# Kernel optimization log

Hardware: AMD Instinct MI355X
Metric: run time of the kernel (lower is better)

The kernel has to match this reference:

```python
import jax, jax.numpy as jnp
import numpy as np

VOCAB, ENC, EMB, DEC, ATT = 10000, 2048, 512, 512, 512
B, P, S = 64, 196, 20
PAD_ID = 0


def setup_inputs() -> dict:
    key = jax.random.key(0)
    ks = jax.random.split(key, 20)
    sc = lambda *sh: 1.0 / np.sqrt(sh[-1])
    def lin(k, out, inp):
        kw, kb = jax.random.split(k)
        s = 1.0 / np.sqrt(inp)
        return (jax.random.uniform(kw, (out, inp), jnp.float32, -s, s),
                jax.random.uniform(kb, (out,), jnp.float32, -s, s))
    wenc_w, wenc_b = lin(ks[0], ATT, ENC)
    wdec_w, wdec_b = lin(ks[1], ATT, DEC)
    V_w, V_b = lin(ks[2], 1, ATT)
    h0_w, h0_b = lin(ks[3], DEC, ENC)
    c0_w, c0_b = lin(ks[4], DEC, ENC)
    W_ih, b_ih = lin(ks[5], 4 * DEC, ENC + EMB)
    W_hh, b_hh = lin(ks[6], 4 * DEC, DEC)
    fc_w, fc_b = lin(ks[7], VOCAB, DEC)
    embed_w = jax.random.normal(ks[8], (VOCAB, EMB), jnp.float32)
    embed_w = embed_w.at[PAD_ID].set(0.0)  # padding_idx row is zero
    image_feat = jax.random.normal(ks[9], (B, P, ENC), jnp.float32)
    captions_ids = jax.random.randint(ks[10], (B, S), 0, VOCAB)
    return dict(image_feat=image_feat, captions_ids=captions_ids,
                wenc_w=wenc_w, wenc_b=wenc_b, wdec_w=wdec_w, wdec_b=wdec_b,
                V_w=V_w, V_b=V_b, embed_w=embed_w,
                h0_w=h0_w, h0_b=h0_b, c0_w=c0_w, c0_b=c0_b,
                W_ih=W_ih, b_ih=b_ih, W_hh=W_hh, b_hh=b_hh,
                fc_w=fc_w, fc_b=fc_b)


def reference(image_feat, captions_ids, wenc_w, wenc_b, wdec_w, wdec_b,
              V_w, V_b, embed_w, h0_w, h0_b, c0_w, c0_b,
              W_ih, b_ih, W_hh, b_hh, fc_w, fc_b):
    # eval mode: no input noise, dropout = identity
    avg = image_feat.mean(axis=1)                                   # [B, ENC]
    h = jax.nn.relu(avg @ h0_w.T + h0_b)                            # [B, DEC]
    c = jax.nn.relu(avg @ c0_w.T + c0_b)
    enc_proj = jnp.einsum('bpe,ae->bpa', image_feat, wenc_w) + wenc_b  # [B,P,ATT]
    emb_seq = embed_w[captions_ids]                                 # [B,S,EMB]
    emb_seq = jnp.transpose(emb_seq, (1, 0, 2))                     # [S,B,EMB]

    def step(carry, emb_t):
        h, c = carry
        att = jnp.tanh(enc_proj + (h @ wdec_w.T + wdec_b)[:, None, :])  # [B,P,ATT]
        e = jnp.einsum('bpa,a->bp', att, V_w[0]) + V_b[0]               # [B,P]
        w = jax.nn.softmax(e, axis=1)
        ctx = jnp.einsum('bp,bpe->be', w, image_feat)                   # [B,ENC]
        x = jnp.concatenate([ctx, emb_t], axis=1)                       # [B,ENC+EMB]
        gates = x @ W_ih.T + b_ih + h @ W_hh.T + b_hh                   # [B,4*DEC]
        i, f, g, o = jnp.split(gates, 4, axis=1)
        c_new = jax.nn.sigmoid(f) * c + jax.nn.sigmoid(i) * jnp.tanh(g)
        h_new = jax.nn.sigmoid(o) * jnp.tanh(c_new)
        logits = h_new @ fc_w.T + fc_b                                  # [B,VOCAB]
        return (h_new, c_new), logits

    _, preds = jax.lax.scan(step, (h, c), emb_seq)                  # [S,B,VOCAB]
    return jnp.transpose(preds, (1, 0, 2))                          # [B,S,VOCAB]
```

## Files before the change

### kernel.cpp

```cpp
#include <hip/hip_runtime.h>
#include <hip/hip_bf16.h>

#define DEV static __device__ __forceinline__

typedef short s16x8 __attribute__((ext_vector_type(8)));
typedef float f32x4 __attribute__((ext_vector_type(4)));
typedef unsigned short u16;

constexpr int Bn = 64, Pn = 196, ENCn = 2048, EMBn = 512, DECn = 512, ATTn = 512;
constexpr int VOCABn = 10000, Sn = 20;

DEV u16 f2bf(float x) {
  union { float f; unsigned u; } v; v.f = x;
  unsigned r = v.u + 0x7fffu + ((v.u >> 16) & 1u);
  return (u16)(r >> 16);
}
DEV float bf2f(u16 b) {
  union { unsigned u; float f; } v; v.u = ((unsigned)b) << 16;
  return v.f;
}
DEV float sigm(float x) { return 1.f / (1.f + __expf(-x)); }
DEV float tanh_fast(float x) {
  float e = __expf(2.f * x);
  return 1.f - 2.f / (e + 1.f);
}

DEV s16x8 ld8(const u16* p) { return *reinterpret_cast<const s16x8*>(p); }
DEV s16x8 ld8(const float* p) {
  s16x8 r;
#pragma unroll
  for (int j = 0; j < 8; j++) r[j] = (short)f2bf(p[j]);
  return r;
}
DEV f32x4 mfma(s16x8 a, s16x8 b, f32x4 c) {
  return __builtin_amdgcn_mfma_f32_16x16x32_bf16(a, b, c, 0, 0, 0);
}

#define GLOAD_LDS16(gsrc, ldst)                                                \
  __builtin_amdgcn_global_load_lds(                                            \
      (const __attribute__((address_space(1))) void*)(gsrc),                   \
      (__attribute__((address_space(3))) void*)(ldst), 16, 0, 0)

__global__ __launch_bounds__(256) void k_cvtfeat_part(
    const float* __restrict__ feat, u16* __restrict__ featbf,
    float* __restrict__ pavg) {
  int b = blockIdx.y, px = blockIdx.x;
  int d8 = threadIdx.x * 8;
  const float* p = feat + ((size_t)b * Pn + px * 28) * ENCn + d8;
  u16* q = featbf + ((size_t)b * Pn + px * 28) * ENCn + d8;
  float acc[8] = {};
  for (int k = 0; k < 28; k++) {
    float4 v0 = *(const float4*)(p + (size_t)k * ENCn);
    float4 v1 = *(const float4*)(p + (size_t)k * ENCn + 4);
    acc[0] += v0.x; acc[1] += v0.y; acc[2] += v0.z; acc[3] += v0.w;
    acc[4] += v1.x; acc[5] += v1.y; acc[6] += v1.z; acc[7] += v1.w;
    s16x8 o;
    o[0] = (short)f2bf(v0.x); o[1] = (short)f2bf(v0.y);
    o[2] = (short)f2bf(v0.z); o[3] = (short)f2bf(v0.w);
    o[4] = (short)f2bf(v1.x); o[5] = (short)f2bf(v1.y);
    o[6] = (short)f2bf(v1.z); o[7] = (short)f2bf(v1.w);
    *(s16x8*)(q + (size_t)k * ENCn) = o;
  }
  float* pp = pavg + ((size_t)px * Bn + b) * ENCn + d8;
  *(f32x4*)pp = f32x4{acc[0], acc[1], acc[2], acc[3]};
  *(f32x4*)(pp + 4) = f32x4{acc[4], acc[5], acc[6], acc[7]};
}

__global__ __launch_bounds__(256) void k_avg_final(
    const float* __restrict__ pavg, float* __restrict__ avg) {
  int idx = blockIdx.x * 256 + threadIdx.x;
  int b = idx >> 9, e4 = (idx & 511) * 4;
  float4 s = {0.f, 0.f, 0.f, 0.f};
#pragma unroll
  for (int px = 0; px < 7; px++) {
    float4 v = *(const float4*)(pavg + ((size_t)px * Bn + b) * ENCn + e4);
    s.x += v.x; s.y += v.y; s.z += v.z; s.w += v.w;
  }
  float4 o = { s.x * (1.f/196.f), s.y * (1.f/196.f), s.z * (1.f/196.f), s.w * (1.f/196.f) };
  *(float4*)(avg + (size_t)b * ENCn + e4) = o;
}

__global__ void k_cvt_all(const float* __restrict__ s0, u16* __restrict__ d0,
                          const float* __restrict__ s1, u16* __restrict__ d1,
                          const float* __restrict__ s2, u16* __restrict__ d2,
                          const float* __restrict__ s3, u16* __restrict__ d3,
                          const float* __restrict__ s4, u16* __restrict__ d4,
                          u16* __restrict__ wdecT) {
  int gid = blockIdx.x * 256 + threadIdx.x, stride = gridDim.x * 256;
  auto run = [&](const float* __restrict__ s, u16* __restrict__ d, int n8) {
    for (int i = gid; i < n8; i += stride) {
      const float4* sp = (const float4*)(s + (size_t)i * 8);
      float4 a = sp[0], b = sp[1];
      s16x8 o;
      o[0] = (short)f2bf(a.x); o[1] = (short)f2bf(a.y);
      o[2] = (short)f2bf(a.z); o[3] = (short)f2bf(a.w);
      o[4] = (short)f2bf(b.x); o[5] = (short)f2bf(b.y);
      o[6] = (short)f2bf(b.z); o[7] = (short)f2bf(b.w);
      *(s16x8*)(d + (size_t)i * 8) = o;
    }
  };
  run(s0, d0, 131072);
  run(s1, d1, 32768);
  run(s2, d2, 655360);
  run(s3, d3, 131072);
  run(s4, d4, 640000);
  for (int i = gid; i < 262144; i += stride) {
    int n = i >> 9, k = i & 511;
    wdecT[(size_t)k * 512 + n] = f2bf(s1[i]);
  }
}

__global__ __launch_bounds__(256) void k_h0c0(
    const float* __restrict__ avg,
    const float* __restrict__ h0w, const float* __restrict__ h0b,
    const float* __restrict__ c0w, const float* __restrict__ c0b,
    u16* __restrict__ h0out, float* __restrict__ c0out,
    float* __restrict__ decpart) {
  int idx = blockIdx.x * 256 + threadIdx.x;
  float* dz = decpart + (size_t)Bn * 512;
#pragma unroll
  for (int j = 0; j < 6; j++) dz[(size_t)j * 16384 + idx] = 0.f;

  int wid = threadIdx.x >> 6, lane = threadIdx.x & 63;
  int r = lane & 15, hi = lane >> 4;
  bool isC = blockIdx.x >= 32;
  int n0 = ((int)blockIdx.x & 31) * 16;
  const float* W = (isC ? c0w : h0w) + (size_t)(n0 + r) * ENCn + hi * 8;
  const float* ap = avg + (size_t)(wid * 16 + r) * ENCn + hi * 8;
  f32x4 acc = {0.f, 0.f, 0.f, 0.f};
  for (int k = 0; k < ENCn; k += 32) acc = mfma(ld8(ap + k), ld8(W + k), acc);
  int col = n0 + r;
  float bb = (isC ? c0b : h0b)[col];
#pragma unroll
  for (int j = 0; j < 4; j++) {
    int row = wid * 16 + hi * 4 + j;
    float v = fmaxf(acc[j] + bb, 0.f);
    if (isC) c0out[(size_t)row * DECn + col] = v;
    else     h0out[(size_t)row * DECn + col] = f2bf(v);
  }
}

template<typename TA, typename TW, int K>
__global__ __launch_bounds__(256) void k_lin64(
    const TA* __restrict__ A, const TW* __restrict__ W,
    const float* __restrict__ bias1, float* __restrict__ outF, size_t ldo) {
  int wid = threadIdx.x >> 6, lane = threadIdx.x & 63;
  int r = lane & 15, hi = lane >> 4;
  int n0 = blockIdx.x * 16;
  const TA* ap = A + (size_t)(wid * 16 + r) * K + hi * 8;
  const TW* wp = W + (size_t)(n0 + r) * K + hi * 8;
  f32x4 acc = {0.f, 0.f, 0.f, 0.f};
  for (int k = 0; k < K; k += 32) acc = mfma(ld8(ap + k), ld8(wp + k), acc);
  int col = n0 + r;
  float bb = bias1 ? bias1[col] : 0.f;
#pragma unroll
  for (int j = 0; j < 4; j++) {
    int row = wid * 16 + hi * 4 + j;
    outF[(size_t)row * ldo + col] = acc[j] + bb;
  }
}

__global__ __launch_bounds__(256) void k_encproj(
    const u16* __restrict__ Abf, const u16* __restrict__ Wbf,
    const float* __restrict__ bias, u16* __restrict__ out) {
  __shared__ u16 As[128][32];
  __shared__ u16 Bs[128][32];
  int tid = threadIdx.x;
  int wid = tid >> 6, lane = tid & 63, r = lane & 15, hi = lane >> 4;
  int wm = wid >> 1, wn = wid & 1;
  int m0 = blockIdx.y * 128, n0 = blockIdx.x * 128;
  int srow = tid >> 2, scol = (tid & 3) * 8;
  const u16* ga = Abf + (size_t)(m0 + srow) * ENCn + scol;
  const u16* gb = Wbf + (size_t)(n0 + srow) * ENCn + scol;
  u16* As1 = &As[0][0];
  u16* Bs1 = &Bs[0][0];
  f32x4 acc[4][4] = {};
  for (int k0 = 0; k0 < ENCn; k0 += 32) {
    GLOAD_LDS16(ga + k0,                      As1 + wid * 512);
    GLOAD_LDS16(ga + k0 + (size_t)64 * ENCn,  As1 + 2048 + wid * 512);
    GLOAD_LDS16(gb + k0,                      Bs1 + wid * 512);
    GLOAD_LDS16(gb + k0 + (size_t)64 * ENCn,  Bs1 + 2048 + wid * 512);
    __syncthreads();
    s16x8 af[4], bfr[4];
#pragma unroll
    for (int i = 0; i < 4; i++) af[i]  = *(const s16x8*)(As1 + (wm * 64 + i * 16 + r) * 32 + hi * 8);
#pragma unroll
    for (int j = 0; j < 4; j++) bfr[j] = *(const s16x8*)(Bs1 + (wn * 64 + j * 16 + r) * 32 + hi * 8);
#pragma unroll
    for (int i = 0; i < 4; i++)
#pragma unroll
      for (int j = 0; j < 4; j++)
        acc[i][j] = mfma(af[i], bfr[j], acc[i][j]);
    __syncthreads();
  }
#pragma unroll
  for (int i = 0; i < 4; i++)
#pragma unroll
    for (int j = 0; j < 4; j++) {
      int col = n0 + wn * 64 + j * 16 + r;
      float bb = bias[col];
#pragma unroll
      for (int q = 0; q < 4; q++) {
        int row = m0 + wm * 64 + i * 16 + hi * 4 + q;
        out[(size_t)row * 512 + col] = f2bf(acc[i][j][q] + bb);
      }
    }
}

__global__ __launch_bounds__(256) void k_gproj(
    const u16* __restrict__ Abf, const u16* __restrict__ Wih,
    u16* __restrict__ G) {
  __shared__ u16 As[128][32];
  __shared__ u16 Bs[128][32];
  int tid = threadIdx.x;
  int wid = tid >> 6, lane = tid & 63, r = lane & 15, hi = lane >> 4;
  int wm = wid >> 1, wn = wid & 1;
  int m0 = blockIdx.y * 128, n0 = blockIdx.x * 128;
  int srow = tid >> 2, scol = (tid & 3) * 8;
  const u16* ga = Abf + (size_t)(m0 + srow) * ENCn + scol;
  int c1 = n0 + srow, c2 = n0 + 64 + srow;
  int w1 = (c1 >> 2) + (c1 & 3) * 512;
  int w2 = (c2 >> 2) + (c2 & 3) * 512;
  const u16* gb1 = Wih + (size_t)w1 * 2560 + scol;
  const u16* gb2 = Wih + (size_t)w2 * 2560 + scol;
  u16* As1 = &As[0][0];
  u16* Bs1 = &Bs[0][0];
  f32x4 acc[4][4] = {};
  for (int k0 = 0; k0 < ENCn; k0 += 32) {
    GLOAD_LDS16(ga + k0,                      As1 + wid * 512);
    GLOAD_LDS16(ga + k0 + (size_t)64 * ENCn,  As1 + 2048 + wid * 512);
    GLOAD_LDS16(gb1 + k0,                     Bs1 + wid * 512);
    GLOAD_LDS16(gb2 + k0,                     Bs1 + 2048 + wid * 512);
    __syncthreads();
    s16x8 af[4], bfr[4];
#pragma unroll
    for (int i = 0; i < 4; i++) af[i]  = *(const s16x8*)(As1 + (wm * 64 + i * 16 + r) * 32 + hi * 8);
#pragma unroll
    for (int j = 0; j < 4; j++) bfr[j] = *(const s16x8*)(Bs1 + (wn * 64 + j * 16 + r) * 32 + hi * 8);
#pragma unroll
    for (int i = 0; i < 4; i++)
#pragma unroll
      for (int j = 0; j < 4; j++)
        acc[i][j] = mfma(af[i], bfr[j], acc[i][j]);
    __syncthreads();
  }
#pragma unroll
  for (int i = 0; i < 4; i++)
#pragma unroll
    for (int j = 0; j < 4; j++) {
      int col = n0 + wn * 64 + j * 16 + r;
#pragma unroll
      for (int q = 0; q < 4; q++) {
        int row = m0 + wm * 64 + i * 16 + hi * 4 + q;
        G[(size_t)row * 2048 + col] = f2bf(acc[i][j][q]);
      }
    }
}

__global__ __launch_bounds__(256) void k_step1(
    const u16* __restrict__ encp, const float* __restrict__ decpart,
    const float* __restrict__ wdecb,
    const float* __restrict__ Vw, const float* __restrict__ Vb,
    float* __restrict__ e_s,
    const float* __restrict__ embw, const int* __restrict__ caps, int t,
    const u16* __restrict__ hin, const u16* __restrict__ Wih,
    const u16* __restrict__ Whh, float* __restrict__ p2) {
  int bx = blockIdx.x, by = blockIdx.y;
  int wid = threadIdx.x >> 6, lane = threadIdx.x & 63;
  if (bx < 49) {
    int p = bx * 4 + wid, b = by;
    int cb = lane * 8;
    float4 dv0 = *(const float4*)(wdecb + cb);
    float4 dv1 = *(const float4*)(wdecb + cb + 4);
#pragma unroll
    for (int q = 0; q < 4; q++) {
      const float* dq = decpart + ((size_t)q * Bn + b) * 512 + cb;
      float4 v0 = *(const float4*)dq, v1 = *(const float4*)(dq + 4);
      dv0.x += v0.x; dv0.y += v0.y; dv0.z += v0.z; dv0.w += v0.w;
      dv1.x += v1.x; dv1.y += v1.y; dv1.z += v1.z; dv1.w += v1.w;
    }
    float4 vv0 = *(const float4*)(Vw + cb), vv1 = *(const float4*)(Vw + cb + 4);
    s16x8 ev = *(const s16x8*)(encp + (((size_t)(b * Pn + p)) << 9) + cb);
    float s = 0.f;
    s += vv0.x * tanh_fast(bf2f((u16)ev[0]) + dv0.x);
    s += vv0.y * tanh_fast(bf2f((u16)ev[1]) + dv0.y);
    s += vv0.z * tanh_fast(bf2f((u16)ev[2]) + dv0.z);
    s += vv0.w * tanh_fast(bf2f((u16)ev[3]) + dv0.w);
    s += vv1.x * tanh_fast(bf2f((u16)ev[4]) + dv1.x);
    s += vv1.y * tanh_fast(bf2f((u16)ev[5]) + dv1.y);
    s += vv1.z * tanh_fast(bf2f((u16)ev[6]) + dv1.z);
    s += vv1.w * tanh_fast(bf2f((u16)ev[7]) + dv1.w);
    for (int m = 32; m; m >>= 1) s += __shfl_xor(s, m);
    if (lane == 0) e_s[(size_t)b * Pn + p] = s + Vb[0];
  } else {
    int sb = (bx - 49) * 64 + by;
    int n0 = sb * 16;
    int r = lane & 15, hi = lane >> 4;
    int brow = wid * 16 + r;
    f32x4 acc = {0.f, 0.f, 0.f, 0.f};
    int id = caps[brow * Sn + t];
    const float* a = embw + (size_t)id * EMBn + hi * 8;
    const u16* w = Wih + (size_t)(n0 + r) * 2560 + 2048 + hi * 8;
#pragma unroll 4
    for (int k = 0; k < 512; k += 32) acc = mfma(ld8(a + k), ld8(w + k), acc);
    const u16* a2 = hin + (size_t)brow * DECn + hi * 8;
    const u16* w2 = Whh + (size_t)(n0 + r) * 512 + hi * 8;
#pragma unroll 4
    for (int k = 0; k < 512; k += 32) acc = mfma(ld8(a2 + k), ld8(w2 + k), acc);
#pragma unroll
    for (int j = 0; j < 4; j++) {
      int row = wid * 16 + hi * 4 + j;
      p2[(size_t)row * 2048 + n0 + r] = acc[j];
    }
  }
}

__global__ __launch_bounds__(256) void k_step2(
    const float* __restrict__ e_s, const u16* __restrict__ G,
    const float* __restrict__ p2, const float* __restrict__ bih,
    const float* __restrict__ bhh, float* __restrict__ cbuf,
    u16* __restrict__ hnew, const u16* __restrict__ wdecT,
    float* __restrict__ decpart) {
  __shared__ float sw[Pn];
  __shared__ float red[256];
  __shared__ float pacc[4 * 512];
  __shared__ float hsh[128];
  int b = blockIdx.y, c = blockIdx.x, tid = threadIdx.x;
  float ev = (tid < Pn) ? e_s[(size_t)b * Pn + tid] : -3.0e38f;
  red[tid] = ev; __syncthreads();
  for (int s = 128; s > 0; s >>= 1) { if (tid < s) red[tid] = fmaxf(red[tid], red[tid + s]); __syncthreads(); }
  float m = red[0]; __syncthreads();
  float ex = (tid < Pn) ? __expf(ev - m) : 0.f;
  red[tid] = ex; __syncthreads();
  for (int s = 128; s > 0; s >>= 1) { if (tid < s) red[tid] += red[tid + s]; __syncthreads(); }
  float inv = 1.f / red[0];
  if (tid < Pn) sw[tid] = ex * inv;
  __syncthreads();
  int g = tid >> 6, t64 = tid & 63;
  int dloc = t64 * 8;
  const u16* gp = G + (size_t)b * Pn * 2048 + c * 512 + dloc;
  float acc[8] = {};
#pragma unroll 4
  for (int p = g; p < Pn; p += 4) {
    float w = sw[p];
    s16x8 v = *(const s16x8*)(gp + (size_t)p * 2048);
#pragma unroll
    for (int j = 0; j < 8; j++) acc[j] += w * bf2f((u16)v[j]);
  }
#pragma unroll
  for (int j = 0; j < 8; j++) pacc[g * 512 + dloc + j] = acc[j];
  __syncthreads();
  if (tid < 128) {
    int d = c * 128 + tid;
    float gv[4];
#pragma unroll
    for (int gg = 0; gg < 4; gg++) {
      int lc = tid * 4 + gg;
      float s = pacc[lc] + pacc[512 + lc] + pacc[1024 + lc] + pacc[1536 + lc];
      int col = gg * 512 + d;
      gv[gg] = s + p2[(size_t)b * 2048 + col] + bih[col] + bhh[col];
    }
    size_t ci = (size_t)b * DECn + d;
    float cn = sigm(gv[1]) * cbuf[ci] + sigm(gv[0]) * tanh_fast(gv[2]);
    float hn = sigm(gv[3]) * tanh_fast(cn);
    cbuf[ci] = cn;
    hnew[ci] = f2bf(hn);
    hsh[tid] = hn;
  }
  __syncthreads();
  float a0 = 0.f, a1 = 0.f;
#pragma unroll 8
  for (int k = 0; k < 128; k++) {
    float h = hsh[k];
    const u16* wr = wdecT + (size_t)(c * 128 + k) * 512;
    a0 += h * bf2f(wr[tid]);
    a1 += h * bf2f(wr[tid + 256]);
  }
  decpart[((size_t)c * Bn + b) * 512 + tid] = a0;
  decpart[((size_t)c * Bn + b) * 512 + tid + 256] = a1;
}

__global__ __launch_bounds__(256) void k_logits(
    const u16* __restrict__ hA, const u16* __restrict__ Wbf,
    const float* __restrict__ bias, float* __restrict__ out) {
  __shared__ u16 As[128][32];
  __shared__ u16 Bs[128][32];
  int tid = threadIdx.x;
  int wid = tid >> 6, lane = tid & 63, r = lane & 15, hi = lane >> 4;
  int wm = wid >> 1, wn = wid & 1;
  int m0 = blockIdx.y * 128, n0 = blockIdx.x * 128;
  int srow = tid >> 2, scol = (tid & 3) * 8;
  const u16* ga = hA + (size_t)(m0 + srow) * 512 + scol;
  int br1 = n0 + srow;       if (br1 > VOCABn - 1) br1 = VOCABn - 1;
  int br2 = n0 + 64 + srow;  if (br2 > VOCABn - 1) br2 = VOCABn - 1;
  const u16* gb1 = Wbf + (size_t)br1 * 512 + scol;
  const u16* gb2 = Wbf + (size_t)br2 * 512 + scol;
  u16* As1 = &As[0][0];
  u16* Bs1 = &Bs[0][0];
  f32x4 acc[4][4] = {};
  for (int k0 = 0; k0 < 512; k0 += 32) {
    GLOAD_LDS16(ga + k0,                     As1 + wid * 512);
    GLOAD_LDS16(ga + k0 + (size_t)64 * 512,  As1 + 2048 + wid * 512);
    GLOAD_LDS16(gb1 + k0,                    Bs1 + wid * 512);
    GLOAD_LDS16(gb2 + k0,                    Bs1 + 2048 + wid * 512);
    __syncthreads();
    s16x8 af[4], bfr[4];
#pragma unroll
    for (int i = 0; i < 4; i++) af[i]  = *(const s16x8*)(As1 + (wm * 64 + i * 16 + r) * 32 + hi * 8);
#pragma unroll
    for (int j = 0; j < 4; j++) bfr[j] = *(const s16x8*)(Bs1 + (wn * 64 + j * 16 + r) * 32 + hi * 8);
#pragma unroll
    for (int i = 0; i < 4; i++)
#pragma unroll
      for (int j = 0; j < 4; j++)
        acc[i][j] = mfma(af[i], bfr[j], acc[i][j]);
    __syncthreads();
  }
#pragma unroll
  for (int i = 0; i < 4; i++)
#pragma unroll
    for (int j = 0; j < 4; j++) {
      int col = n0 + wn * 64 + j * 16 + r;
      if (col < VOCABn) {
        float bb = bias[col];
#pragma unroll
        for (int q = 0; q < 4; q++) {
          int row = m0 + wm * 64 + i * 16 + hi * 4 + q;
          int tt = row >> 6, b = row & 63;
          out[((size_t)b * Sn + tt) * VOCABn + col] = acc[i][j][q] + bb;
        }
      }
    }
}

extern "C" void kernel_launch(void* const* d_in, const int* in_sizes, int n_in,
                              void* d_out, int out_size, void* d_ws, size_t ws_size,
                              hipStream_t stream) {
  const float* image_feat = (const float*)d_in[0];
  const int*   captions   = (const int*)d_in[1];
  const float* wenc_w = (const float*)d_in[2];
  const float* wenc_b = (const float*)d_in[3];
  const float* wdec_w = (const float*)d_in[4];
  const float* wdec_b = (const float*)d_in[5];
  const float* V_w    = (const float*)d_in[6];
  const float* V_b    = (const float*)d_in[7];
  const float* embed_w = (const float*)d_in[8];
  const float* h0_w = (const float*)d_in[9];
  const float* h0_b = (const float*)d_in[10];
  const float* c0_w = (const float*)d_in[11];
  const float* c0_b = (const float*)d_in[12];
  const float* W_ih = (const float*)d_in[13];
  const float* b_ih = (const float*)d_in[14];
  const float* W_hh = (const float*)d_in[15];
  const float* b_hh = (const float*)d_in[16];
  const float* fc_w = (const float*)d_in[17];
  const float* fc_b = (const float*)d_in[18];
  float* out = (float*)d_out;

  char* w = (char*)d_ws;
  auto alloc = [&](size_t bytes) { void* p = (void*)w; w += (bytes + 255) & ~(size_t)255; return p; };
  u16* if_bf   = (u16*)alloc(sizeof(u16) * (size_t)Bn * Pn * ENCn);
  u16* Gbuf    = (u16*)alloc(sizeof(u16) * (size_t)Bn * Pn * 2048);
  u16* wenc_bf = (u16*)alloc(sizeof(u16) * (size_t)ATTn * ENCn);
  u16* wdec_bf = (u16*)alloc(sizeof(u16) * (size_t)ATTn * DECn);
  u16* wdecT   = (u16*)alloc(sizeof(u16) * (size_t)DECn * DECn);
  u16* Wih_bf  = (u16*)alloc(sizeof(u16) * (size_t)2048 * 2560);
  u16* Whh_bf  = (u16*)alloc(sizeof(u16) * (size_t)2048 * 512);
  u16* fcw_bf  = (u16*)alloc(sizeof(u16) * (size_t)VOCABn * DECn);
  u16* hall    = (u16*)alloc(sizeof(u16) * (size_t)(Sn + 1) * Bn * DECn);
  u16* encp    = (u16*)alloc(sizeof(u16) * (size_t)Bn * Pn * ATTn);
  float* avg   = (float*)alloc(sizeof(float) * (size_t)Bn * ENCn);
  float* pavg  = (float*)alloc(sizeof(float) * (size_t)7 * Bn * ENCn);
  float* e_s   = (float*)alloc(sizeof(float) * (size_t)Bn * Pn);
  float* cbuf  = (float*)alloc(sizeof(float) * (size_t)Bn * DECn);
  float* p2    = (float*)alloc(sizeof(float) * (size_t)Bn * 2048);
  float* decpart = (float*)alloc(sizeof(float) * (size_t)4 * Bn * 512);

  k_cvtfeat_part<<<dim3(7, Bn), 256, 0, stream>>>(image_feat, if_bf, pavg);
  k_avg_final<<<128, 256, 0, stream>>>(pavg, avg);
  k_cvt_all<<<2048, 256, 0, stream>>>(wenc_w, wenc_bf, wdec_w, wdec_bf,
                                      W_ih, Wih_bf, W_hh, Whh_bf, fc_w, fcw_bf,
                                      wdecT);
  k_encproj<<<dim3(4, 98), 256, 0, stream>>>(if_bf, wenc_bf, wenc_b, encp);
  k_gproj<<<dim3(16, 98), 256, 0, stream>>>(if_bf, Wih_bf, Gbuf);
  k_h0c0<<<64, 256, 0, stream>>>(avg, h0_w, h0_b, c0_w, c0_b, hall, cbuf, decpart);
  k_lin64<u16, u16, 512><<<32, 256, 0, stream>>>(hall, wdec_bf, nullptr, decpart, 512);

  for (int t = 0; t < Sn; t++) {
    const u16* hin = hall + (size_t)t * Bn * DECn;
    u16* hnew = hall + (size_t)(t + 1) * Bn * DECn;
    k_step1<<<dim3(51, Bn), 256, 0, stream>>>(encp, decpart, wdec_b, V_w, V_b, e_s,
                                              embed_w, captions, t, hin,
                                              Wih_bf, Whh_bf, p2);
    k_step2<<<dim3(4, Bn), 256, 0, stream>>>(e_s, Gbuf, p2, b_ih, b_hh, cbuf,
                                             hnew, wdecT, decpart);
  }
  k_logits<<<dim3(79, 10), 256, 0, stream>>>(hall + (size_t)Bn * DECn, fcw_bf, fc_b, out);
}
```

Measured before the change: 1.112 ms.

## Hoist embedding gate projection, merge big GEMMs, swizzle LDS, widen step2 blocks

The embedding-to-gates projection is moved out of the per-step kernel into one batched GEMM over all timesteps, fed by a bf16 copy of the embedding table. The encoder-projection and gate-projection GEMMs are merged into a single launch. LDS reads in the GEMMs use an XOR swizzle to cut bank conflicts. The feature-conversion kernel uses more blocks with fewer rows each, and step2 runs 512 threads with an 8-way split of the context reduction. These changes shorten the serial recurrent loop and the prologue, at the cost of an extra fp32 buffer for all steps and extra weight conversion.

```diff
diff --git a/kernel.cpp b/kernel.cpp
--- a/kernel.cpp
+++ b/kernel.cpp
@@ -26,12 +26,6 @@
 }
 
 DEV s16x8 ld8(const u16* p) { return *reinterpret_cast<const s16x8*>(p); }
-DEV s16x8 ld8(const float* p) {
-  s16x8 r;
-#pragma unroll
-  for (int j = 0; j < 8; j++) r[j] = (short)f2bf(p[j]);
-  return r;
-}
 DEV f32x4 mfma(s16x8 a, s16x8 b, f32x4 c) {
   return __builtin_amdgcn_mfma_f32_16x16x32_bf16(a, b, c, 0, 0, 0);
 }
@@ -46,10 +40,11 @@
     float* __restrict__ pavg) {
   int b = blockIdx.y, px = blockIdx.x;
   int d8 = threadIdx.x * 8;
-  const float* p = feat + ((size_t)b * Pn + px * 28) * ENCn + d8;
-  u16* q = featbf + ((size_t)b * Pn + px * 28) * ENCn + d8;
+  const float* p = feat + ((size_t)b * Pn + px * 7) * ENCn + d8;
+  u16* q = featbf + ((size_t)b * Pn + px * 7) * ENCn + d8;
   float acc[8] = {};
-  for (int k = 0; k < 28; k++) {
+#pragma unroll
+  for (int k = 0; k < 7; k++) {
     float4 v0 = *(const float4*)(p + (size_t)k * ENCn);
     float4 v1 = *(const float4*)(p + (size_t)k * ENCn + 4);
     acc[0] += v0.x; acc[1] += v0.y; acc[2] += v0.z; acc[3] += v0.w;
@@ -72,7 +67,7 @@
   int b = idx >> 9, e4 = (idx & 511) * 4;
   float4 s = {0.f, 0.f, 0.f, 0.f};
 #pragma unroll
-  for (int px = 0; px < 7; px++) {
+  for (int px = 0; px < 28; px++) {
     float4 v = *(const float4*)(pavg + ((size_t)px * Bn + b) * ENCn + e4);
     s.x += v.x; s.y += v.y; s.z += v.z; s.w += v.w;
   }
@@ -85,6 +80,7 @@
                           const float* __restrict__ s2, u16* __restrict__ d2,
                           const float* __restrict__ s3, u16* __restrict__ d3,
                           const float* __restrict__ s4, u16* __restrict__ d4,
+                          const float* __restrict__ s5, u16* __restrict__ d5,
                           u16* __restrict__ wdecT) {
   int gid = blockIdx.x * 256 + threadIdx.x, stride = gridDim.x * 256;
   auto run = [&](const float* __restrict__ s, u16* __restrict__ d, int n8) {
@@ -104,6 +100,7 @@
   run(s2, d2, 655360);
   run(s3, d3, 131072);
   run(s4, d4, 640000);
+  run(s5, d5, 640000);
   for (int i = gid; i < 262144; i += stride) {
     int n = i >> 9, k = i & 511;
     wdecT[(size_t)k * 512 + n] = f2bf(s1[i]);
@@ -128,7 +125,12 @@
   const float* W = (isC ? c0w : h0w) + (size_t)(n0 + r) * ENCn + hi * 8;
   const float* ap = avg + (size_t)(wid * 16 + r) * ENCn + hi * 8;
   f32x4 acc = {0.f, 0.f, 0.f, 0.f};
-  for (int k = 0; k < ENCn; k += 32) acc = mfma(ld8(ap + k), ld8(W + k), acc);
+  for (int k = 0; k < ENCn; k += 32) {
+    s16x8 af, wf;
+#pragma unroll
+    for (int j = 0; j < 8; j++) { af[j] = (short)f2bf(ap[k + j]); wf[j] = (short)f2bf(W[k + j]); }
+    acc = mfma(af, wf, acc);
+  }
   int col = n0 + r;
   float bb = (isC ? c0b : h0b)[col];
 #pragma unroll
@@ -160,71 +162,35 @@
   }
 }
 
-__global__ __launch_bounds__(256) void k_encproj(
-    const u16* __restrict__ Abf, const u16* __restrict__ Wbf,
-    const float* __restrict__ bias, u16* __restrict__ out) {
+__global__ __launch_bounds__(256) void k_bigproj(
+    const u16* __restrict__ Abf, const u16* __restrict__ Wih,
+    const u16* __restrict__ Wenc, const float* __restrict__ encb,
+    u16* __restrict__ G, u16* __restrict__ encp) {
   __shared__ u16 As[128][32];
   __shared__ u16 Bs[128][32];
   int tid = threadIdx.x;
   int wid = tid >> 6, lane = tid & 63, r = lane & 15, hi = lane >> 4;
   int wm = wid >> 1, wn = wid & 1;
-  int m0 = blockIdx.y * 128, n0 = blockIdx.x * 128;
-  int srow = tid >> 2, scol = (tid & 3) * 8;
+  int m0 = blockIdx.y * 128;
+  bool isG = blockIdx.x < 16;
+  int n0 = (isG ? (int)blockIdx.x : (int)blockIdx.x - 16) * 128;
+  int srow = tid >> 2;
+  int scol = (((tid & 3) ^ (srow & 3))) * 8;
   const u16* ga = Abf + (size_t)(m0 + srow) * ENCn + scol;
-  const u16* gb = Wbf + (size_t)(n0 + srow) * ENCn + scol;
+  const u16 *gb1, *gb2;
+  if (isG) {
+    int c1 = n0 + srow, c2 = n0 + 64 + srow;
+    int w1 = (c1 >> 2) + (c1 & 3) * 512;
+    int w2 = (c2 >> 2) + (c2 & 3) * 512;
+    gb1 = Wih + (size_t)w1 * 2560 + scol;
+    gb2 = Wih + (size_t)w2 * 2560 + scol;
+  } else {
+    gb1 = Wenc + (size_t)(n0 + srow) * ENCn + scol;
+    gb2 = Wenc + (size_t)(n0 + 64 + srow) * ENCn + scol;
+  }
   u16* As1 = &As[0][0];
   u16* Bs1 = &Bs[0][0];
-  f32x4 acc[4][4] = {};
-  for (int k0 = 0; k0 < ENCn; k0 += 32) {
-    GLOAD_LDS16(ga + k0,                      As1 + wid * 512);
-    GLOAD_LDS16(ga + k0 + (size_t)64 * ENCn,  As1 + 2048 + wid * 512);
-    GLOAD_LDS16(gb + k0,                      Bs1 + wid * 512);
-    GLOAD_LDS16(gb + k0 + (size_t)64 * ENCn,  Bs1 + 2048 + wid * 512);
-    __syncthreads();
-    s16x8 af[4], bfr[4];
-#pragma unroll
-    for (int i = 0; i < 4; i++) af[i]  = *(const s16x8*)(As1 + (wm * 64 + i * 16 + r) * 32 + hi * 8);
-#pragma unroll
-    for (int j = 0; j < 4; j++) bfr[j] = *(const s16x8*)(Bs1 + (wn * 64 + j * 16 + r) * 32 + hi * 8);
-#pragma unroll
-    for (int i = 0; i < 4; i++)
-#pragma unroll
-      for (int j = 0; j < 4; j++)
-        acc[i][j] = mfma(af[i], bfr[j], acc[i][j]);
-    __syncthreads();
-  }
-#pragma unroll
-  for (int i = 0; i < 4; i++)
-#pragma unroll
-    for (int j = 0; j < 4; j++) {
-      int col = n0 + wn * 64 + j * 16 + r;
-      float bb = bias[col];
-#pragma unroll
-      for (int q = 0; q < 4; q++) {
-        int row = m0 + wm * 64 + i * 16 + hi * 4 + q;
-        out[(size_t)row * 512 + col] = f2bf(acc[i][j][q] + bb);
-      }
-    }
-}
-
-__global__ __launch_bounds__(256) void k_gproj(
-    const u16* __restrict__ Abf, const u16* __restrict__ Wih,
-    u16* __restrict__ G) {
-  __shared__ u16 As[128][32];
-  __shared__ u16 Bs[128][32];
-  int tid = threadIdx.x;
-  int wid = tid >> 6, lane = tid & 63, r = lane & 15, hi = lane >> 4;
-  int wm = wid >> 1, wn = wid & 1;
-  int m0 = blockIdx.y * 128, n0 = blockIdx.x * 128;
-  int srow = tid >> 2, scol = (tid & 3) * 8;
-  const u16* ga = Abf + (size_t)(m0 + srow) * ENCn + scol;
-  int c1 = n0 + srow, c2 = n0 + 64 + srow;
-  int w1 = (c1 >> 2) + (c1 & 3) * 512;
-  int w2 = (c2 >> 2) + (c2 & 3) * 512;
-  const u16* gb1 = Wih + (size_t)w1 * 2560 + scol;
-  const u16* gb2 = Wih + (size_t)w2 * 2560 + scol;
-  u16* As1 = &As[0][0];
-  u16* Bs1 = &Bs[0][0];
+  int sa = (hi ^ (r & 3)) * 8;
   f32x4 acc[4][4] = {};
   for (int k0 = 0; k0 < ENCn; k0 += 32) {
     GLOAD_LDS16(ga + k0,                      As1 + wid * 512);
@@ -234,9 +200,9 @@
     __syncthreads();
     s16x8 af[4], bfr[4];
 #pragma unroll
-    for (int i = 0; i < 4; i++) af[i]  = *(const s16x8*)(As1 + (wm * 64 + i * 16 + r) * 32 + hi * 8);
-#pragma unroll
-    for (int j = 0; j < 4; j++) bfr[j] = *(const s16x8*)(Bs1 + (wn * 64 + j * 16 + r) * 32 + hi * 8);
+    for (int i = 0; i < 4; i++) af[i]  = *(const s16x8*)(As1 + (wm * 64 + i * 16 + r) * 32 + sa);
+#pragma unroll
+    for (int j = 0; j < 4; j++) bfr[j] = *(const s16x8*)(Bs1 + (wn * 64 + j * 16 + r) * 32 + sa);
 #pragma unroll
     for (int i = 0; i < 4; i++)
 #pragma unroll
@@ -252,7 +218,61 @@
 #pragma unroll
       for (int q = 0; q < 4; q++) {
         int row = m0 + wm * 64 + i * 16 + hi * 4 + q;
-        G[(size_t)row * 2048 + col] = f2bf(acc[i][j][q]);
+        if (isG) G[(size_t)row * 2048 + col] = f2bf(acc[i][j][q]);
+        else     encp[(size_t)row * 512 + col] = f2bf(acc[i][j][q] + encb[col]);
+      }
+    }
+}
+
+__global__ __launch_bounds__(256) void k_eproj(
+    const u16* __restrict__ embbf, const int* __restrict__ caps,
+    const u16* __restrict__ Wih, float* __restrict__ E) {
+  __shared__ u16 As[128][32];
+  __shared__ u16 Bs[128][32];
+  int tid = threadIdx.x;
+  int wid = tid >> 6, lane = tid & 63, r = lane & 15, hi = lane >> 4;
+  int wm = wid >> 1, wn = wid & 1;
+  int m0 = blockIdx.y * 128, n0 = blockIdx.x * 128;
+  int srow = tid >> 2;
+  int scol = (((tid & 3) ^ (srow & 3))) * 8;
+  int row1 = m0 + srow, row2 = row1 + 64;
+  int id1 = caps[(row1 & 63) * Sn + (row1 >> 6)];
+  int id2 = caps[(row2 & 63) * Sn + (row2 >> 6)];
+  const u16* ga1 = embbf + (size_t)id1 * 512 + scol;
+  const u16* ga2 = embbf + (size_t)id2 * 512 + scol;
+  const u16* gb1 = Wih + (size_t)(n0 + srow) * 2560 + 2048 + scol;
+  const u16* gb2 = Wih + (size_t)(n0 + 64 + srow) * 2560 + 2048 + scol;
+  u16* As1 = &As[0][0];
+  u16* Bs1 = &Bs[0][0];
+  int sa = (hi ^ (r & 3)) * 8;
+  f32x4 acc[4][4] = {};
+  for (int k0 = 0; k0 < 512; k0 += 32) {
+    GLOAD_LDS16(ga1 + k0, As1 + wid * 512);
+    GLOAD_LDS16(ga2 + k0, As1 + 2048 + wid * 512);
+    GLOAD_LDS16(gb1 + k0, Bs1 + wid * 512);
+    GLOAD_LDS16(gb2 + k0, Bs1 + 2048 + wid * 512);
+    __syncthreads();
+    s16x8 af[4], bfr[4];
+#pragma unroll
+    for (int i = 0; i < 4; i++) af[i]  = *(const s16x8*)(As1 + (wm * 64 + i * 16 + r) * 32 + sa);
+#pragma unroll
+    for (int j = 0; j < 4; j++) bfr[j] = *(const s16x8*)(Bs1 + (wn * 64 + j * 16 + r) * 32 + sa);
+#pragma unroll
+    for (int i = 0; i < 4; i++)
+#pragma unroll
+      for (int j = 0; j < 4; j++)
+        acc[i][j] = mfma(af[i], bfr[j], acc[i][j]);
+    __syncthreads();
+  }
+#pragma unroll
+  for (int i = 0; i < 4; i++)
+#pragma unroll
+    for (int j = 0; j < 4; j++) {
+      int col = n0 + wn * 64 + j * 16 + r;
+#pragma unroll
+      for (int q = 0; q < 4; q++) {
+        int row = m0 + wm * 64 + i * 16 + hi * 4 + q;
+        E[(size_t)row * 2048 + col] = acc[i][j][q];
       }
     }
 }
@@ -262,9 +282,8 @@
     const float* __restrict__ wdecb,
     const float* __restrict__ Vw, const float* __restrict__ Vb,
     float* __restrict__ e_s,
-    const float* __restrict__ embw, const int* __restrict__ caps, int t,
-    const u16* __restrict__ hin, const u16* __restrict__ Wih,
-    const u16* __restrict__ Whh, float* __restrict__ p2) {
+    const u16* __restrict__ hin, const u16* __restrict__ Whh,
+    float* __restrict__ p2) {
   int bx = blockIdx.x, by = blockIdx.y;
   int wid = threadIdx.x >> 6, lane = threadIdx.x & 63;
   if (bx < 49) {
@@ -298,11 +317,6 @@
     int r = lane & 15, hi = lane >> 4;
     int brow = wid * 16 + r;
     f32x4 acc = {0.f, 0.f, 0.f, 0.f};
-    int id = caps[brow * Sn + t];
-    const float* a = embw + (size_t)id * EMBn + hi * 8;
-    const u16* w = Wih + (size_t)(n0 + r) * 2560 + 2048 + hi * 8;
-#pragma unroll 4
-    for (int k = 0; k < 512; k += 32) acc = mfma(ld8(a + k), ld8(w + k), acc);
     const u16* a2 = hin + (size_t)brow * DECn + hi * 8;
     const u16* w2 = Whh + (size_t)(n0 + r) * 512 + hi * 8;
 #pragma unroll 4
@@ -315,24 +329,24 @@
   }
 }
 
-__global__ __launch_bounds__(256) void k_step2(
+__global__ __launch_bounds__(512) void k_step2(
     const float* __restrict__ e_s, const u16* __restrict__ G,
-    const float* __restrict__ p2, const float* __restrict__ bih,
-    const float* __restrict__ bhh, float* __restrict__ cbuf,
-    u16* __restrict__ hnew, const u16* __restrict__ wdecT,
-    float* __restrict__ decpart) {
+    const float* __restrict__ p2, const float* __restrict__ Et,
+    const float* __restrict__ bih, const float* __restrict__ bhh,
+    float* __restrict__ cbuf, u16* __restrict__ hnew,
+    const u16* __restrict__ wdecT, float* __restrict__ decpart) {
   __shared__ float sw[Pn];
-  __shared__ float red[256];
-  __shared__ float pacc[4 * 512];
+  __shared__ float red[512];
+  __shared__ float pacc[8 * 512];
   __shared__ float hsh[128];
   int b = blockIdx.y, c = blockIdx.x, tid = threadIdx.x;
   float ev = (tid < Pn) ? e_s[(size_t)b * Pn + tid] : -3.0e38f;
   red[tid] = ev; __syncthreads();
-  for (int s = 128; s > 0; s >>= 1) { if (tid < s) red[tid] = fmaxf(red[tid], red[tid + s]); __syncthreads(); }
+  for (int s = 256; s > 0; s >>= 1) { if (tid < s) red[tid] = fmaxf(red[tid], red[tid + s]); __syncthreads(); }
   float m = red[0]; __syncthreads();
   float ex = (tid < Pn) ? __expf(ev - m) : 0.f;
   red[tid] = ex; __syncthreads();
-  for (int s = 128; s > 0; s >>= 1) { if (tid < s) red[tid] += red[tid + s]; __syncthreads(); }
+  for (int s = 256; s > 0; s >>= 1) { if (tid < s) red[tid] += red[tid + s]; __syncthreads(); }
   float inv = 1.f / red[0];
   if (tid < Pn) sw[tid] = ex * inv;
   __syncthreads();
@@ -340,15 +354,15 @@
   int dloc = t64 * 8;
   const u16* gp = G + (size_t)b * Pn * 2048 + c * 512 + dloc;
   float acc[8] = {};
-#pragma unroll 4
-  for (int p = g; p < Pn; p += 4) {
+#pragma unroll 2
+  for (int p = g; p < Pn; p += 8) {
     float w = sw[p];
     s16x8 v = *(const s16x8*)(gp + (size_t)p * 2048);
 #pragma unroll
     for (int j = 0; j < 8; j++) acc[j] += w * bf2f((u16)v[j]);
   }
 #pragma unroll
-  for (int j = 0; j < 8; j++) pacc[g * 512 + dloc + j] = acc[j];
+  for (int j = 0; j < 8; j++) pacc[g * 512 + j * 64 + t64] = acc[j];
   __syncthreads();
   if (tid < 128) {
     int d = c * 128 + tid;
@@ -356,9 +370,13 @@
 #pragma unroll
     for (int gg = 0; gg < 4; gg++) {
       int lc = tid * 4 + gg;
-      float s = pacc[lc] + pacc[512 + lc] + pacc[1024 + lc] + pacc[1536 + lc];
+      int ia = (lc & 7) * 64 + (lc >> 3);
+      float s = 0.f;
+#pragma unroll
+      for (int gr = 0; gr < 8; gr++) s += pacc[gr * 512 + ia];
       int col = gg * 512 + d;
-      gv[gg] = s + p2[(size_t)b * 2048 + col] + bih[col] + bhh[col];
+      gv[gg] = s + p2[(size_t)b * 2048 + col] + Et[(size_t)b * 2048 + col]
+             + bih[col] + bhh[col];
     }
     size_t ci = (size_t)b * DECn + d;
     float cn = sigm(gv[1]) * cbuf[ci] + sigm(gv[0]) * tanh_fast(gv[2]);
@@ -368,16 +386,11 @@
     hsh[tid] = hn;
   }
   __syncthreads();
-  float a0 = 0.f, a1 = 0.f;
+  float a0 = 0.f;
 #pragma unroll 8
-  for (int k = 0; k < 128; k++) {
-    float h = hsh[k];
-    const u16* wr = wdecT + (size_t)(c * 128 + k) * 512;
-    a0 += h * bf2f(wr[tid]);
-    a1 += h * bf2f(wr[tid + 256]);
-  }
+  for (int k = 0; k < 128; k++)
+    a0 += hsh[k] * bf2f(wdecT[(size_t)(c * 128 + k) * 512 + tid]);
   decpart[((size_t)c * Bn + b) * 512 + tid] = a0;
-  decpart[((size_t)c * Bn + b) * 512 + tid + 256] = a1;
 }
 
 __global__ __launch_bounds__(256) void k_logits(
@@ -389,7 +402,8 @@
   int wid = tid >> 6, lane = tid & 63, r = lane & 15, hi = lane >> 4;
   int wm = wid >> 1, wn = wid & 1;
   int m0 = blockIdx.y * 128, n0 = blockIdx.x * 128;
-  int srow = tid >> 2, scol = (tid & 3) * 8;
+  int srow = tid >> 2;
+  int scol = (((tid & 3) ^ (srow & 3))) * 8;
   const u16* ga = hA + (size_t)(m0 + srow) * 512 + scol;
   int br1 = n0 + srow;       if (br1 > VOCABn - 1) br1 = VOCABn - 1;
   int br2 = n0 + 64 + srow;  if (br2 > VOCABn - 1) br2 = VOCABn - 1;
@@ -397,6 +411,7 @@
   const u16* gb2 = Wbf + (size_t)br2 * 512 + scol;
   u16* As1 = &As[0][0];
   u16* Bs1 = &Bs[0][0];
+  int sa = (hi ^ (r & 3)) * 8;
   f32x4 acc[4][4] = {};
   for (int k0 = 0; k0 < 512; k0 += 32) {
     GLOAD_LDS16(ga + k0,                     As1 + wid * 512);
@@ -406,9 +421,9 @@
     __syncthreads();
     s16x8 af[4], bfr[4];
 #pragma unroll
-    for (int i = 0; i < 4; i++) af[i]  = *(const s16x8*)(As1 + (wm * 64 + i * 16 + r) * 32 + hi * 8);
-#pragma unroll
-    for (int j = 0; j < 4; j++) bfr[j] = *(const s16x8*)(Bs1 + (wn * 64 + j * 16 + r) * 32 + hi * 8);
+    for (int i = 0; i < 4; i++) af[i]  = *(const s16x8*)(As1 + (wm * 64 + i * 16 + r) * 32 + sa);
+#pragma unroll
+    for (int j = 0; j < 4; j++) bfr[j] = *(const s16x8*)(Bs1 + (wn * 64 + j * 16 + r) * 32 + sa);
 #pragma unroll
     for (int i = 0; i < 4; i++)
 #pragma unroll
@@ -467,22 +482,25 @@
   u16* Wih_bf  = (u16*)alloc(sizeof(u16) * (size_t)2048 * 2560);
   u16* Whh_bf  = (u16*)alloc(sizeof(u16) * (size_t)2048 * 512);
   u16* fcw_bf  = (u16*)alloc(sizeof(u16) * (size_t)VOCABn * DECn);
+  u16* emb_bf  = (u16*)alloc(sizeof(u16) * (size_t)VOCABn * EMBn);
   u16* hall    = (u16*)alloc(sizeof(u16) * (size_t)(Sn + 1) * Bn * DECn);
   u16* encp    = (u16*)alloc(sizeof(u16) * (size_t)Bn * Pn * ATTn);
+  float* Ebuf  = (float*)alloc(sizeof(float) * (size_t)Sn * Bn * 2048);
   float* avg   = (float*)alloc(sizeof(float) * (size_t)Bn * ENCn);
-  float* pavg  = (float*)alloc(sizeof(float) * (size_t)7 * Bn * ENCn);
+  float* pavg  = (float*)alloc(sizeof(float) * (size_t)28 * Bn * ENCn);
   float* e_s   = (float*)alloc(sizeof(float) * (size_t)Bn * Pn);
   float* cbuf  = (float*)alloc(sizeof(float) * (size_t)Bn * DECn);
   float* p2    = (float*)alloc(sizeof(float) * (size_t)Bn * 2048);
   float* decpart = (float*)alloc(sizeof(float) * (size_t)4 * Bn * 512);
 
-  k_cvtfeat_part<<<dim3(7, Bn), 256, 0, stream>>>(image_feat, if_bf, pavg);
+  k_cvtfeat_part<<<dim3(28, Bn), 256, 0, stream>>>(image_feat, if_bf, pavg);
   k_avg_final<<<128, 256, 0, stream>>>(pavg, avg);
   k_cvt_all<<<2048, 256, 0, stream>>>(wenc_w, wenc_bf, wdec_w, wdec_bf,
                                       W_ih, Wih_bf, W_hh, Whh_bf, fc_w, fcw_bf,
-                                      wdecT);
-  k_encproj<<<dim3(4, 98), 256, 0, stream>>>(if_bf, wenc_bf, wenc_b, encp);
-  k_gproj<<<dim3(16, 98), 256, 0, stream>>>(if_bf, Wih_bf, Gbuf);
+                                      embed_w, emb_bf, wdecT);
+  k_bigproj<<<dim3(20, 98), 256, 0, stream>>>(if_bf, Wih_bf, wenc_bf, wenc_b,
+                                              Gbuf, encp);
+  k_eproj<<<dim3(16, 10), 256, 0, stream>>>(emb_bf, captions, Wih_bf, Ebuf);
   k_h0c0<<<64, 256, 0, stream>>>(avg, h0_w, h0_b, c0_w, c0_b, hall, cbuf, decpart);
   k_lin64<u16, u16, 512><<<32, 256, 0, stream>>>(hall, wdec_bf, nullptr, decpart, 512);
 
@@ -490,10 +508,10 @@
     const u16* hin = hall + (size_t)t * Bn * DECn;
     u16* hnew = hall + (size_t)(t + 1) * Bn * DECn;
     k_step1<<<dim3(51, Bn), 256, 0, stream>>>(encp, decpart, wdec_b, V_w, V_b, e_s,
-                                              embed_w, captions, t, hin,
-                                              Wih_bf, Whh_bf, p2);
-    k_step2<<<dim3(4, Bn), 256, 0, stream>>>(e_s, Gbuf, p2, b_ih, b_hh, cbuf,
-                                             hnew, wdecT, decpart);
+                                              hin, Whh_bf, p2);
+    k_step2<<<dim3(4, Bn), 512, 0, stream>>>(e_s, Gbuf, p2,
+                                             Ebuf + (size_t)t * Bn * 2048,
+                                             b_ih, b_hh, cbuf, hnew, wdecT, decpart);
   }
   k_logits<<<dim3(79, 10), 256, 0, stream>>>(hall + (size_t)Bn * DECn, fcw_bf, fc_b, out);
 }
```

Result: faster. 990.2 us (-11.0%).
